# Optimization experiments

Hardware: AMD Instinct MI355X
Metric: run time of the kernel (lower is better)

Reference implementation:

```python
import jax, jax.numpy as jnp
import numpy as np

DIM_IN = 768
DIM_OUT = 64
SEQ = 4096
BATCH = 4

def setup_inputs() -> dict:
    key = jax.random.key(0)
    ks = jax.random.split(key, 7)
    s = 1.0 / np.sqrt(DIM_IN)
    return {
        "x": jax.random.normal(ks[0], (BATCH, SEQ, DIM_IN), dtype=jnp.float32),
        "wq": jax.random.uniform(ks[1], (DIM_IN, DIM_OUT), jnp.float32, -s, s),
        "bq": jax.random.uniform(ks[2], (DIM_OUT,), jnp.float32, -s, s),
        "wk": jax.random.uniform(ks[3], (DIM_IN, DIM_OUT), jnp.float32, -s, s),
        "bk": jax.random.uniform(ks[4], (DIM_OUT,), jnp.float32, -s, s),
        "wv": jax.random.uniform(ks[5], (DIM_IN, DIM_OUT), jnp.float32, -s, s),
        "bv": jax.random.uniform(ks[6], (DIM_OUT,), jnp.float32, -s, s),
    }

def reference(x, wq, bq, wk, bk, wv, bv):
    # QKV projections: (B, S, D_in) @ (D_in, D_out) + bias
    q = x @ wq + bq
    k = x @ wk + bk
    v = x @ wv + bv
    # full causal attention, scores scaled by sqrt(d_out) AFTER masking (as in source)
    scores = jnp.einsum('bqd,bkd->bqk', q, k)  # (B, S, S)
    seq = x.shape[1]
    causal = jnp.tril(jnp.ones((seq, seq), dtype=bool))  # True = keep
    scores = jnp.where(causal, scores, -jnp.inf)
    scale = 1.0 / np.sqrt(k.shape[-1]).astype(np.float32)
    weights = jax.nn.softmax(scores * scale, axis=-1)
    # dropout_rate = 0.0 -> identity
    return jnp.einsum('bqk,bkd->bqd', weights, v)
```

## Files before the change

### kernel.cpp

```cpp
#include <hip/hip_runtime.h>
#include <hip/hip_bf16.h>

#define BATCH 4
#define SEQ   4096
#define DIN   768
#define DOUT  64

typedef __attribute__((ext_vector_type(4))) float f32x4;
typedef __attribute__((ext_vector_type(8))) short short8;
typedef __attribute__((ext_vector_type(4))) short short4v;

#define QSCALE 0.18033688011112043f

static __device__ __forceinline__ unsigned short f2bf(float f) {
    union { float f; unsigned u; } un; un.f = f;
    unsigned r = un.u + 0x7FFF + ((un.u >> 16) & 1);
    return (unsigned short)(r >> 16);
}
static __device__ __forceinline__ float bf2f(unsigned short h) {
    union { unsigned u; float f; } un; un.u = ((unsigned)h) << 16;
    return un.f;
}
static __device__ __forceinline__ unsigned packbf(float lo, float hi) {
    return ((unsigned)f2bf(hi) << 16) | (unsigned)f2bf(lo);
}

__global__ void wprep_kernel(const float* __restrict__ wq,
                             const float* __restrict__ wk,
                             const float* __restrict__ wv,
                             unsigned short* __restrict__ wF) {
    __shared__ float lds[64][65];
    int o = blockIdx.x / 12, kt = blockIdx.x % 12;
    const float* w = (o == 0) ? wq : (o == 1) ? wk : wv;
    int tid = threadIdx.x;
    int k0 = kt * 64;
    #pragma unroll
    for (int i = 0; i < 16; ++i) {
        int flat = tid + i * 256;
        int kl = flat >> 6, n = flat & 63;
        lds[kl][n] = w[(k0 + kl) * 64 + n];
    }
    __syncthreads();
    int lane = tid & 63;
    int m = lane & 15, g = lane >> 4;
    #pragma unroll
    for (int i = 0; i < 2; ++i) {
        int f = i * 4 + (tid >> 6);
        int t = f >> 1, kcl = f & 1;
        int kc = kt * 2 + kcl;
        int nc = o * 4 + t;
        short8 v;
        #pragma unroll
        for (int j = 0; j < 8; ++j)
            v[j] = (short)f2bf(lds[kcl * 32 + g * 8 + j][t * 16 + m]);
        *(short8*)&wF[(size_t)(nc * 24 + kc) * 512 + lane * 8] = v;
    }
}

__global__ void __launch_bounds__(256) proj_kernel(
        const float* __restrict__ x,
        const float* __restrict__ bq,
        const float* __restrict__ bk,
        const float* __restrict__ bv,
        const unsigned short* __restrict__ wF,
        unsigned short* __restrict__ Qf,
        unsigned short* __restrict__ Kf,
        unsigned short* __restrict__ Vf) {
    __shared__ __align__(16) unsigned short xs[32][776];
    __shared__ unsigned short tr[4][16][24];

    int tid = threadIdx.x;
    int w = tid >> 6;
    int lane = tid & 63;
    int m = lane & 15, g = lane >> 4;
    int r0 = blockIdx.x * 32;

    {
        const float* xbase = x + (size_t)r0 * DIN;
        #pragma unroll
        for (int i = 0; i < 24; ++i) {
            int flat4 = tid + i * 256;
            int row = flat4 / 192;
            int c4 = flat4 - row * 192;
            float4 v = *(const float4*)(xbase + (size_t)row * DIN + c4 * 4);
            short4v sv;
            sv[0] = (short)f2bf(v.x); sv[1] = (short)f2bf(v.y);
            sv[2] = (short)f2bf(v.z); sv[3] = (short)f2bf(v.w);
            *(short4v*)&xs[row][c4 * 4] = sv;
        }
    }
    __syncthreads();

    f32x4 acc[2][3];
    #pragma unroll
    for (int st = 0; st < 2; ++st)
        #pragma unroll
        for (int t = 0; t < 3; ++t) acc[st][t] = (f32x4){0.f, 0.f, 0.f, 0.f};

    for (int kc = 0; kc < 24; ++kc) {
        short8 af0 = *(const short8*)&xs[m][kc * 32 + g * 8];
        short8 af1 = *(const short8*)&xs[16 + m][kc * 32 + g * 8];
        #pragma unroll
        for (int tt = 0; tt < 3; ++tt) {
            int nc = w * 3 + tt;
            short8 bfrg = *(const short8*)(wF + (size_t)(nc * 24 + kc) * 512 + lane * 8);
            acc[0][tt] = __builtin_amdgcn_mfma_f32_16x16x32_bf16(af0, bfrg, acc[0][tt], 0, 0, 0);
            acc[1][tt] = __builtin_amdgcn_mfma_f32_16x16x32_bf16(af1, bfrg, acc[1][tt], 0, 0, 0);
        }
    }

    int b2 = r0 >> 12;
    int s = (r0 & 4095) >> 5;
    #pragma unroll
    for (int st = 0; st < 2; ++st) {
        #pragma unroll
        for (int tt = 0; tt < 3; ++tt) {
            int nc = w * 3 + tt;
            int o = nc >> 2;
            int t = nc & 3;
            const float* bias_p = (o == 0) ? bq : (o == 1) ? bk : bv;
            float bias = bias_p[t * 16 + m];
            #pragma unroll
            for (int r = 0; r < 4; ++r) {
                float val = acc[st][tt][r] + bias;
                if (o == 0) val *= QSCALE;
                tr[w][g * 4 + r][m] = f2bf(val);
            }
            if (o < 2) {
                if (g < 2) {
                    short8 v8;
                    #pragma unroll
                    for (int j = 0; j < 8; ++j) v8[j] = (short)tr[w][m][g * 8 + j];
                    unsigned short* dst = (o == 0) ? Qf : Kf;
                    int c = t >> 1;
                    *(short8*)&dst[(size_t)((blockIdx.x * 2 + st) * 2 + c) * 512
                                   + (((t & 1) * 2 + g) * 16 + m) * 8] = v8;
                }
            } else {
                if (g < 2) {
                    short8 v8;
                    #pragma unroll
                    for (int j = 0; j < 8; ++j) v8[j] = (short)tr[w][g * 8 + j][m];
                    *(short8*)&Vf[((size_t)(b2 * 128 + s) * 4 + t) * 512
                                  + ((st * 2 + g) * 16 + m) * 8] = v8;
                }
            }
        }
    }
}

__global__ void __launch_bounds__(512, 2) attn_kernel(
        const unsigned short* __restrict__ Qf,
        const unsigned short* __restrict__ Kf,
        const unsigned short* __restrict__ Vf,
        float* __restrict__ out) {
    __shared__ __align__(16) unsigned short pacc[8][16][68];
    __shared__ float pm[8][16];
    __shared__ float pl[8][16];

    int j = blockIdx.x;
    int b = j & 3;
    int qt = j >> 2;
    int base0 = qt * 16;
    int base1 = (255 - qt) * 16;
    int ns0 = (qt + 2) >> 1;
    int ns1 = (257 - qt) >> 1;
    int tid = threadIdx.x;
    int w = tid >> 6;
    int lane = tid & 63;
    int m = lane & 15, g = lane >> 4;

    const unsigned short* Q0 = Qf + (size_t)(b * 256 + qt) * 1024 + lane * 8;
    const unsigned short* Q1 = Qf + (size_t)(b * 256 + 255 - qt) * 1024 + lane * 8;
    short8 qf00 = *(const short8*)(Q0);
    short8 qf01 = *(const short8*)(Q0 + 512);
    short8 qf10 = *(const short8*)(Q1);
    short8 qf11 = *(const short8*)(Q1 + 512);

    f32x4 acc[2][4];
    #pragma unroll
    for (int rt = 0; rt < 2; ++rt)
        #pragma unroll
        for (int t = 0; t < 4; ++t) acc[rt][t] = (f32x4){0.f, 0.f, 0.f, 0.f};
    float mrun0 = -INFINITY, mrun1 = -INFINITY;
    float lsum0 = 0.f, lsum1 = 0.f;

    const unsigned short* Kbase = Kf + (size_t)(b * 256) * 1024 + lane * 8;
    const unsigned short* Vbase = Vf + (size_t)(b * 128) * 2048 + lane * 8;

    int srcA = m + 16 * ((g & 1) * 2);
    int srcB = srcA + 16;
    bool hi = (g >= 2);

    short8 kf[4], vf[4];
    if (w < ns1) {
        #pragma unroll
        for (int t = 0; t < 4; ++t) {
            kf[t] = *(const short8*)(Kbase + (size_t)w * 2048 + t * 512);
            vf[t] = *(const short8*)(Vbase + (size_t)w * 2048 + t * 512);
        }
    }

    for (int s = w; s < ns1; s += 8) {
        int kv0 = s * 32;
        int sn = s + 8;
        bool have = (sn < ns1);
        bool do0 = (s < ns0);

        if (do0) {
            f32x4 st0 = (f32x4){0.f, 0.f, 0.f, 0.f};
            f32x4 st1 = (f32x4){0.f, 0.f, 0.f, 0.f};
            st0 = __builtin_amdgcn_mfma_f32_16x16x32_bf16(kf[0], qf00, st0, 0, 0, 0);
            st0 = __builtin_amdgcn_mfma_f32_16x16x32_bf16(kf[1], qf01, st0, 0, 0, 0);
            st1 = __builtin_amdgcn_mfma_f32_16x16x32_bf16(kf[2], qf00, st1, 0, 0, 0);
            st1 = __builtin_amdgcn_mfma_f32_16x16x32_bf16(kf[3], qf01, st1, 0, 0, 0);
            if (s == ns0 - 1) {
                int q = base0 + m;
                #pragma unroll
                for (int r = 0; r < 4; ++r) {
                    if (kv0 + g * 4 + r > q)      st0[r] = -INFINITY;
                    if (kv0 + 16 + g * 4 + r > q) st1[r] = -INFINITY;
                }
            }
            float th = mrun0 + 8.0f;
            bool need = (st0[0] > th) | (st0[1] > th) | (st0[2] > th) | (st0[3] > th)
                      | (st1[0] > th) | (st1[1] > th) | (st1[2] > th) | (st1[3] > th);
            if (__any(need)) {
                float rmax = fmaxf(fmaxf(fmaxf(st0[0], st0[1]), fmaxf(st0[2], st0[3])),
                                   fmaxf(fmaxf(st1[0], st1[1]), fmaxf(st1[2], st1[3])));
                rmax = fmaxf(rmax, __shfl_xor(rmax, 16));
                rmax = fmaxf(rmax, __shfl_xor(rmax, 32));
                float mnew = fmaxf(mrun0, rmax);
                float alpha = __builtin_amdgcn_exp2f(mrun0 - mnew);
                mrun0 = mnew;
                lsum0 *= alpha;
                #pragma unroll
                for (int t = 0; t < 4; ++t)
                    #pragma unroll
                    for (int r = 0; r < 4; ++r) acc[0][t][r] *= alpha;
            }
            float p00 = __builtin_amdgcn_exp2f(st0[0] - mrun0);
            float p01 = __builtin_amdgcn_exp2f(st0[1] - mrun0);
            float p02 = __builtin_amdgcn_exp2f(st0[2] - mrun0);
            float p03 = __builtin_amdgcn_exp2f(st0[3] - mrun0);
            float p10 = __builtin_amdgcn_exp2f(st1[0] - mrun0);
            float p11 = __builtin_amdgcn_exp2f(st1[1] - mrun0);
            float p12 = __builtin_amdgcn_exp2f(st1[2] - mrun0);
            float p13 = __builtin_amdgcn_exp2f(st1[3] - mrun0);
            float ssum = ((p00 + p01) + (p02 + p03)) + ((p10 + p11) + (p12 + p13));
            ssum += __shfl_xor(ssum, 16);
            ssum += __shfl_xor(ssum, 32);
            lsum0 += ssum;
            unsigned d0 = packbf(p00, p01), d1 = packbf(p02, p03);
            unsigned d2 = packbf(p10, p11), d3 = packbf(p12, p13);
            unsigned a0 = __shfl(d0, srcA), a1 = __shfl(d1, srcA);
            unsigned a2 = __shfl(d2, srcA), a3 = __shfl(d3, srcA);
            unsigned b0 = __shfl(d0, srcB), b1 = __shfl(d1, srcB);
            unsigned b2 = __shfl(d2, srcB), b3 = __shfl(d3, srcB);
            union { unsigned u[4]; short8 s8; } pb;
            pb.u[0] = hi ? a2 : a0; pb.u[1] = hi ? a3 : a1;
            pb.u[2] = hi ? b2 : b0; pb.u[3] = hi ? b3 : b1;
            #pragma unroll
            for (int t = 0; t < 4; ++t)
                acc[0][t] = __builtin_amdgcn_mfma_f32_16x16x32_bf16(vf[t], pb.s8, acc[0][t], 0, 0, 0);
        }

        {
            f32x4 st0 = (f32x4){0.f, 0.f, 0.f, 0.f};
            f32x4 st1 = (f32x4){0.f, 0.f, 0.f, 0.f};
            st0 = __builtin_amdgcn_mfma_f32_16x16x32_bf16(kf[0], qf10, st0, 0, 0, 0);
            st0 = __builtin_amdgcn_mfma_f32_16x16x32_bf16(kf[1], qf11, st0, 0, 0, 0);
            st1 = __builtin_amdgcn_mfma_f32_16x16x32_bf16(kf[2], qf10, st1, 0, 0, 0);
            st1 = __builtin_amdgcn_mfma_f32_16x16x32_bf16(kf[3], qf11, st1, 0, 0, 0);

            if (have) {
                #pragma unroll
                for (int t = 0; t < 4; ++t)
                    kf[t] = *(const short8*)(Kbase + (size_t)sn * 2048 + t * 512);
            }

            if (s == ns1 - 1) {
                int q = base1 + m;
                #pragma unroll
                for (int r = 0; r < 4; ++r) {
                    if (kv0 + g * 4 + r > q)      st0[r] = -INFINITY;
                    if (kv0 + 16 + g * 4 + r > q) st1[r] = -INFINITY;
                }
            }
            float th = mrun1 + 8.0f;
            bool need = (st0[0] > th) | (st0[1] > th) | (st0[2] > th) | (st0[3] > th)
                      | (st1[0] > th) | (st1[1] > th) | (st1[2] > th) | (st1[3] > th);
            if (__any(need)) {
                float rmax = fmaxf(fmaxf(fmaxf(st0[0], st0[1]), fmaxf(st0[2], st0[3])),
                                   fmaxf(fmaxf(st1[0], st1[1]), fmaxf(st1[2], st1[3])));
                rmax = fmaxf(rmax, __shfl_xor(rmax, 16));
                rmax = fmaxf(rmax, __shfl_xor(rmax, 32));
                float mnew = fmaxf(mrun1, rmax);
                float alpha = __builtin_amdgcn_exp2f(mrun1 - mnew);
                mrun1 = mnew;
                lsum1 *= alpha;
                #pragma unroll
                for (int t = 0; t < 4; ++t)
                    #pragma unroll
                    for (int r = 0; r < 4; ++r) acc[1][t][r] *= alpha;
            }
            float p00 = __builtin_amdgcn_exp2f(st0[0] - mrun1);
            float p01 = __builtin_amdgcn_exp2f(st0[1] - mrun1);
            float p02 = __builtin_amdgcn_exp2f(st0[2] - mrun1);
            float p03 = __builtin_amdgcn_exp2f(st0[3] - mrun1);
            float p10 = __builtin_amdgcn_exp2f(st1[0] - mrun1);
            float p11 = __builtin_amdgcn_exp2f(st1[1] - mrun1);
            float p12 = __builtin_amdgcn_exp2f(st1[2] - mrun1);
            float p13 = __builtin_amdgcn_exp2f(st1[3] - mrun1);
            float ssum = ((p00 + p01) + (p02 + p03)) + ((p10 + p11) + (p12 + p13));
            ssum += __shfl_xor(ssum, 16);
            ssum += __shfl_xor(ssum, 32);
            lsum1 += ssum;
            unsigned d0 = packbf(p00, p01), d1 = packbf(p02, p03);
            unsigned d2 = packbf(p10, p11), d3 = packbf(p12, p13);
            unsigned a0 = __shfl(d0, srcA), a1 = __shfl(d1, srcA);
            unsigned a2 = __shfl(d2, srcA), a3 = __shfl(d3, srcA);
            unsigned b0 = __shfl(d0, srcB), b1 = __shfl(d1, srcB);
            unsigned b2 = __shfl(d2, srcB), b3 = __shfl(d3, srcB);
            union { unsigned u[4]; short8 s8; } pb;
            pb.u[0] = hi ? a2 : a0; pb.u[1] = hi ? a3 : a1;
            pb.u[2] = hi ? b2 : b0; pb.u[3] = hi ? b3 : b1;
            #pragma unroll
            for (int t = 0; t < 4; ++t)
                acc[1][t] = __builtin_amdgcn_mfma_f32_16x16x32_bf16(vf[t], pb.s8, acc[1][t], 0, 0, 0);

            if (have) {
                #pragma unroll
                for (int t = 0; t < 4; ++t)
                    vf[t] = *(const short8*)(Vbase + (size_t)sn * 2048 + t * 512);
            }
        }
    }

    #pragma unroll
    for (int rt = 0; rt < 2; ++rt) {
        int qbase = (rt == 0) ? base0 : base1;
        float mr = (rt == 0) ? mrun0 : mrun1;
        float ls = (rt == 0) ? lsum0 : lsum1;
        if (lane < 16) {
            pm[w][m] = mr;
            pl[w][m] = ls;
        }
        #pragma unroll
        for (int t = 0; t < 4; ++t)
            #pragma unroll
            for (int r = 0; r < 4; ++r)
                pacc[w][m][t * 16 + g * 4 + r] = f2bf(acc[rt][t][r]);
        __syncthreads();

        if (tid < 256) {
            int row = tid >> 4;
            int c4 = (tid & 15) * 4;
            float mmax = pm[0][row];
            #pragma unroll
            for (int w2 = 1; w2 < 8; ++w2) mmax = fmaxf(mmax, pm[w2][row]);
            float lt = 0.f;
            float o0 = 0.f, o1 = 0.f, o2 = 0.f, o3 = 0.f;
            #pragma unroll
            for (int w2 = 0; w2 < 8; ++w2) {
                float sc2 = __builtin_amdgcn_exp2f(pm[w2][row] - mmax);
                lt += pl[w2][row] * sc2;
                short4v pa4 = *(const short4v*)&pacc[w2][row][c4];
                o0 += bf2f((unsigned short)pa4[0]) * sc2;
                o1 += bf2f((unsigned short)pa4[1]) * sc2;
                o2 += bf2f((unsigned short)pa4[2]) * sc2;
                o3 += bf2f((unsigned short)pa4[3]) * sc2;
            }
            float invl = 1.0f / lt;
            float4 res = make_float4(o0 * invl, o1 * invl, o2 * invl, o3 * invl);
            *(float4*)&out[(size_t)(b * SEQ + qbase + row) * DOUT + c4] = res;
        }
        __syncthreads();
    }
}

extern "C" void kernel_launch(void* const* d_in, const int* in_sizes, int n_in,
                              void* d_out, int out_size, void* d_ws, size_t ws_size,
                              hipStream_t stream) {
    const float* x  = (const float*)d_in[0];
    const float* wq = (const float*)d_in[1];
    const float* bq = (const float*)d_in[2];
    const float* wk = (const float*)d_in[3];
    const float* bk = (const float*)d_in[4];
    const float* wv = (const float*)d_in[5];
    const float* bv = (const float*)d_in[6];
    float* out = (float*)d_out;

    char* ws = (char*)d_ws;
    unsigned short* wF = (unsigned short*)ws;
    unsigned short* Qf = (unsigned short*)(ws + 294912);
    unsigned short* Kf = (unsigned short*)(ws + 294912 + 2097152);
    unsigned short* Vf = (unsigned short*)(ws + 294912 + 4194304);

    wprep_kernel<<<36, 256, 0, stream>>>(wq, wk, wv, wF);
    proj_kernel<<<512, 256, 0, stream>>>(x, bq, bk, bv, wF, Qf, Kf, Vf);
    attn_kernel<<<512, 512, 0, stream>>>(Qf, Kf, Vf, out);
}
```

Measured before the change: 49.47 us.

## Compute softmax row sums via MFMA with ones and transpose P through LDS

Drops the per-tile cross-lane shuffle reduction of the softmax denominator. Instead an extra MFMA multiplies P by a ones matrix, so the row sums build up in a fifth accumulator that gets the same alpha rescale as the output. It also replaces the shuffle-based register transpose of P with a write and read through a per-wave LDS scratch buffer. This costs one extra MFMA and more accumulator registers per tile. The row sums are now taken from the bf16-rounded P values, and the LDS round trip relies on wave-local ordering without an explicit barrier.

```diff
diff --git a/kernel.cpp b/kernel.cpp
--- a/kernel.cpp
+++ b/kernel.cpp
@@ -9,6 +9,7 @@
 typedef __attribute__((ext_vector_type(4))) float f32x4;
 typedef __attribute__((ext_vector_type(8))) short short8;
 typedef __attribute__((ext_vector_type(4))) short short4v;
+typedef __attribute__((ext_vector_type(2))) unsigned uint2v;
 
 #define QSCALE 0.18033688011112043f
 
@@ -154,6 +155,7 @@
         const unsigned short* __restrict__ Kf,
         const unsigned short* __restrict__ Vf,
         float* __restrict__ out) {
+    __shared__ __align__(16) unsigned short PT[8][16][40];
     __shared__ __align__(16) unsigned short pacc[8][16][68];
     __shared__ float pm[8][16];
     __shared__ float pl[8][16];
@@ -177,20 +179,19 @@
     short8 qf10 = *(const short8*)(Q1);
     short8 qf11 = *(const short8*)(Q1 + 512);
 
-    f32x4 acc[2][4];
+    short8 onesA;
+    #pragma unroll
+    for (int jj = 0; jj < 8; ++jj) onesA[jj] = (short)0x3F80;
+
+    f32x4 acc[2][5];
     #pragma unroll
     for (int rt = 0; rt < 2; ++rt)
         #pragma unroll
-        for (int t = 0; t < 4; ++t) acc[rt][t] = (f32x4){0.f, 0.f, 0.f, 0.f};
+        for (int t = 0; t < 5; ++t) acc[rt][t] = (f32x4){0.f, 0.f, 0.f, 0.f};
     float mrun0 = -INFINITY, mrun1 = -INFINITY;
-    float lsum0 = 0.f, lsum1 = 0.f;
 
     const unsigned short* Kbase = Kf + (size_t)(b * 256) * 1024 + lane * 8;
     const unsigned short* Vbase = Vf + (size_t)(b * 128) * 2048 + lane * 8;
-
-    int srcA = m + 16 * ((g & 1) * 2);
-    int srcB = srcA + 16;
-    bool hi = (g >= 2);
 
     short8 kf[4], vf[4];
     if (w < ns1) {
@@ -233,9 +234,8 @@
                 float mnew = fmaxf(mrun0, rmax);
                 float alpha = __builtin_amdgcn_exp2f(mrun0 - mnew);
                 mrun0 = mnew;
-                lsum0 *= alpha;
-                #pragma unroll
-                for (int t = 0; t < 4; ++t)
+                #pragma unroll
+                for (int t = 0; t < 5; ++t)
                     #pragma unroll
                     for (int r = 0; r < 4; ++r) acc[0][t][r] *= alpha;
             }
@@ -247,22 +247,13 @@
             float p11 = __builtin_amdgcn_exp2f(st1[1] - mrun0);
             float p12 = __builtin_amdgcn_exp2f(st1[2] - mrun0);
             float p13 = __builtin_amdgcn_exp2f(st1[3] - mrun0);
-            float ssum = ((p00 + p01) + (p02 + p03)) + ((p10 + p11) + (p12 + p13));
-            ssum += __shfl_xor(ssum, 16);
-            ssum += __shfl_xor(ssum, 32);
-            lsum0 += ssum;
-            unsigned d0 = packbf(p00, p01), d1 = packbf(p02, p03);
-            unsigned d2 = packbf(p10, p11), d3 = packbf(p12, p13);
-            unsigned a0 = __shfl(d0, srcA), a1 = __shfl(d1, srcA);
-            unsigned a2 = __shfl(d2, srcA), a3 = __shfl(d3, srcA);
-            unsigned b0 = __shfl(d0, srcB), b1 = __shfl(d1, srcB);
-            unsigned b2 = __shfl(d2, srcB), b3 = __shfl(d3, srcB);
-            union { unsigned u[4]; short8 s8; } pb;
-            pb.u[0] = hi ? a2 : a0; pb.u[1] = hi ? a3 : a1;
-            pb.u[2] = hi ? b2 : b0; pb.u[3] = hi ? b3 : b1;
+            *(uint2v*)&PT[w][m][g * 4]      = (uint2v){packbf(p00, p01), packbf(p02, p03)};
+            *(uint2v*)&PT[w][m][16 + g * 4] = (uint2v){packbf(p10, p11), packbf(p12, p13)};
+            short8 pb = *(const short8*)&PT[w][m][g * 8];
             #pragma unroll
             for (int t = 0; t < 4; ++t)
-                acc[0][t] = __builtin_amdgcn_mfma_f32_16x16x32_bf16(vf[t], pb.s8, acc[0][t], 0, 0, 0);
+                acc[0][t] = __builtin_amdgcn_mfma_f32_16x16x32_bf16(vf[t], pb, acc[0][t], 0, 0, 0);
+            acc[0][4] = __builtin_amdgcn_mfma_f32_16x16x32_bf16(onesA, pb, acc[0][4], 0, 0, 0);
         }
 
         {
@@ -298,9 +289,8 @@
                 float mnew = fmaxf(mrun1, rmax);
                 float alpha = __builtin_amdgcn_exp2f(mrun1 - mnew);
                 mrun1 = mnew;
-                lsum1 *= alpha;
-                #pragma unroll
-                for (int t = 0; t < 4; ++t)
+                #pragma unroll
+                for (int t = 0; t < 5; ++t)
                     #pragma unroll
                     for (int r = 0; r < 4; ++r) acc[1][t][r] *= alpha;
             }
@@ -312,22 +302,13 @@
             float p11 = __builtin_amdgcn_exp2f(st1[1] - mrun1);
             float p12 = __builtin_amdgcn_exp2f(st1[2] - mrun1);
             float p13 = __builtin_amdgcn_exp2f(st1[3] - mrun1);
-            float ssum = ((p00 + p01) + (p02 + p03)) + ((p10 + p11) + (p12 + p13));
-            ssum += __shfl_xor(ssum, 16);
-            ssum += __shfl_xor(ssum, 32);
-            lsum1 += ssum;
-            unsigned d0 = packbf(p00, p01), d1 = packbf(p02, p03);
-            unsigned d2 = packbf(p10, p11), d3 = packbf(p12, p13);
-            unsigned a0 = __shfl(d0, srcA), a1 = __shfl(d1, srcA);
-            unsigned a2 = __shfl(d2, srcA), a3 = __shfl(d3, srcA);
-            unsigned b0 = __shfl(d0, srcB), b1 = __shfl(d1, srcB);
-            unsigned b2 = __shfl(d2, srcB), b3 = __shfl(d3, srcB);
-            union { unsigned u[4]; short8 s8; } pb;
-            pb.u[0] = hi ? a2 : a0; pb.u[1] = hi ? a3 : a1;
-            pb.u[2] = hi ? b2 : b0; pb.u[3] = hi ? b3 : b1;
+            *(uint2v*)&PT[w][m][g * 4]      = (uint2v){packbf(p00, p01), packbf(p02, p03)};
+            *(uint2v*)&PT[w][m][16 + g * 4] = (uint2v){packbf(p10, p11), packbf(p12, p13)};
+            short8 pb = *(const short8*)&PT[w][m][g * 8];
             #pragma unroll
             for (int t = 0; t < 4; ++t)
-                acc[1][t] = __builtin_amdgcn_mfma_f32_16x16x32_bf16(vf[t], pb.s8, acc[1][t], 0, 0, 0);
+                acc[1][t] = __builtin_amdgcn_mfma_f32_16x16x32_bf16(vf[t], pb, acc[1][t], 0, 0, 0);
+            acc[1][4] = __builtin_amdgcn_mfma_f32_16x16x32_bf16(onesA, pb, acc[1][4], 0, 0, 0);
 
             if (have) {
                 #pragma unroll
@@ -341,10 +322,9 @@
     for (int rt = 0; rt < 2; ++rt) {
         int qbase = (rt == 0) ? base0 : base1;
         float mr = (rt == 0) ? mrun0 : mrun1;
-        float ls = (rt == 0) ? lsum0 : lsum1;
         if (lane < 16) {
             pm[w][m] = mr;
-            pl[w][m] = ls;
+            pl[w][m] = acc[rt][4][0];
         }
         #pragma unroll
         for (int t = 0; t < 4; ++t)
```

Result: no change. 49.13 us (-0.7%).
